# Kernel optimization log

Measured on AMD Instinct MI355X. Metric: run time of the kernel, lower is better.

Reference implementation:

```python
import jax, jax.numpy as jnp
import numpy as np


def setup_inputs() -> dict:
    key = jax.random.key(0)
    k1, k2, k3, k4 = jax.random.split(key, 4)
    b, s, h, z = 4, 4096, 2048, 64
    scale = 1.0 / np.sqrt(h)
    return {
        "hidden_states": jax.random.normal(k1, (b, s, h), dtype=jnp.float32),
        # nn.Linear(h, z, bias=False): store as (h, z) so y = x @ W
        "Wq": jax.random.normal(k2, (h, z), dtype=jnp.float32) * scale,
        "Wk": jax.random.normal(k3, (h, z), dtype=jnp.float32) * scale,
        "Wv": jax.random.normal(k4, (h, z), dtype=jnp.float32) * scale,
    }


def reference(hidden_states, Wq, Wk, Wv):
    b, s, h = hidden_states.shape
    z = Wq.shape[1]
    # Three small projections: (b, s, z), cast to float32 as in original
    q = jnp.einsum("bsh,hz->bsz", hidden_states, Wq).astype(jnp.float32)
    k = jnp.einsum("bsh,hz->bsz", hidden_states, Wk).astype(jnp.float32)
    v = jnp.einsum("bsh,hz->bsz", hidden_states, Wv).astype(jnp.float32)
    # Per-token outer product over the expert dim: (b, s, z, z)
    attn = q[..., :, None] * k[..., None, :]
    attn = jax.nn.softmax(attn, axis=-1)
    # Weighted sum over the key expert axis j: out[..., i] = sum_j attn[..., i, j] * v[..., j]
    out = jnp.einsum("bsij,bsj->bsi", attn, v)
    return out.reshape(b * s, z)
```

## Files before the change

### kernel.cpp

```cpp
#include <hip/hip_runtime.h>


typedef __bf16 bf16x8 __attribute__((ext_vector_type(8)));
typedef float f32x4  __attribute__((ext_vector_type(4)));

#define NTOK   16384
#define HDIM   2048
#define NCHUNK 64
#define KCH    32
#define CH_STRIDE (12 * 2 * 512)

#define SWZ(row, kq) ((kq) ^ ((row) & 7))

#define GLOAD_LDS16(g, l)                                                      \
  __builtin_amdgcn_global_load_lds(                                            \
      (const __attribute__((address_space(1))) void*)(g),                      \
      (__attribute__((address_space(3))) void*)(l), 16, 0, 0)

#define WAITV7 asm volatile("s_waitcnt vmcnt(7)" ::: "memory")
#define WAITV0 asm volatile("s_waitcnt vmcnt(0)" ::: "memory")
#define SBAR   __builtin_amdgcn_s_barrier()
#define SCHEDB __builtin_amdgcn_sched_barrier(0)

__global__ void pack_w_kernel(const float* __restrict__ Wq,
                              const float* __restrict__ Wk,
                              const float* __restrict__ Wv,
                              __bf16* __restrict__ bfrag)
{
  int u = blockIdx.x * blockDim.x + threadIdx.x;
  if (u >= NCHUNK * 12 * 64) return;
  int l  = u & 63;
  int tn = (u >> 6) % 12;
  int c  = u / (12 * 64);
  int n  = tn * 16 + (l & 15);
  int kb = c * 32 + ((l >> 4) << 3);
  const float* W = (n < 64) ? Wq : (n < 128) ? Wk : Wv;
  int nn = n & 63;
  bf16x8 hi, lo;
#pragma unroll
  for (int j = 0; j < 8; ++j) {
    float f = W[(size_t)(kb + j) * 64 + nn];
    __bf16 h = (__bf16)f;
    hi[j] = h;
    lo[j] = (__bf16)(f - (float)h);
  }
  size_t base = (size_t)(c * 12 + tn) * 1024 + (size_t)l * 8;
  *(bf16x8*)(bfrag + base)       = hi;
  *(bf16x8*)(bfrag + base + 512) = lo;
}

#define ASMLOADB(S, cc)                                                        \
  {                                                                            \
    const __bf16* nbp  = bp + (size_t)(cc) * CH_STRIDE;                        \
    const __bf16* nbp4 = nbp + 2048;                                           \
    asm volatile("global_load_dwordx4 %0, %1, off"                             \
                 : "=&v"(S##h[0]) : "v"(nbp)  : "memory");                     \
    asm volatile("global_load_dwordx4 %0, %1, off offset:1024"                 \
                 : "=&v"(S##l[0]) : "v"(nbp)  : "memory");                     \
    asm volatile("global_load_dwordx4 %0, %1, off offset:2048"                 \
                 : "=&v"(S##h[1]) : "v"(nbp)  : "memory");                     \
    asm volatile("global_load_dwordx4 %0, %1, off offset:3072"                 \
                 : "=&v"(S##l[1]) : "v"(nbp)  : "memory");                     \
    asm volatile("global_load_dwordx4 %0, %1, off"                             \
                 : "=&v"(S##h[2]) : "v"(nbp4) : "memory");                     \
    asm volatile("global_load_dwordx4 %0, %1, off offset:1024"                 \
                 : "=&v"(S##l[2]) : "v"(nbp4) : "memory");                     \
  }

#define COMPUTE(ab, S)                                                         \
  {                                                                            \
    const int r0 = mr, r1 = 16 + mr;                                           \
    float4 A[4];                                                               \
    A[0] = *(const float4*)&(ab)[r0 * 32 + SWZ(r0, 2 * quad)     * 4];         \
    A[1] = *(const float4*)&(ab)[r0 * 32 + SWZ(r0, 2 * quad + 1) * 4];         \
    A[2] = *(const float4*)&(ab)[r1 * 32 + SWZ(r1, 2 * quad)     * 4];         \
    A[3] = *(const float4*)&(ab)[r1 * 32 + SWZ(r1, 2 * quad + 1) * 4];         \
    bf16x8 ah[2], al[2];                                                       \
    _Pragma("unroll")                                                          \
    for (int i = 0; i < 2; ++i) {                                              \
      float av[8] = {A[2*i].x, A[2*i].y, A[2*i].z, A[2*i].w,                   \
                     A[2*i+1].x, A[2*i+1].y, A[2*i+1].z, A[2*i+1].w};          \
      _Pragma("unroll")                                                        \
      for (int j = 0; j < 8; ++j) {                                            \
        __bf16 h = (__bf16)av[j];                                              \
        ah[i][j] = h;                                                          \
        al[i][j] = (__bf16)(av[j] - (float)h);                                 \
      }                                                                        \
    }                                                                          \
    _Pragma("unroll")                                                          \
    for (int i = 0; i < 2; ++i)                                                \
      _Pragma("unroll")                                                        \
      for (int t = 0; t < 3; ++t) {                                            \
        acc[i][t] = __builtin_amdgcn_mfma_f32_16x16x32_bf16(ah[i], S##h[t], acc[i][t], 0, 0, 0); \
        acc[i][t] = __builtin_amdgcn_mfma_f32_16x16x32_bf16(al[i], S##h[t], acc[i][t], 0, 0, 0); \
        acc[i][t] = __builtin_amdgcn_mfma_f32_16x16x32_bf16(ah[i], S##l[t], acc[i][t], 0, 0, 0); \
      }                                                                        \
  }

__global__ __launch_bounds__(512, 4) void router_kernel(
    const float* __restrict__ x,
    const __bf16* __restrict__ bfrag,
    float* __restrict__ out)
{
  const int tok0 = blockIdx.x * 32;
  const int w    = threadIdx.x >> 6;
  const int lane = threadIdx.x & 63;
  const int kh   = w >> 2;
  const int wc   = w & 3;
  const int mr   = lane & 15;
  const int quad = lane >> 4;

  __shared__ float qkv[2][32 * 196];
  __shared__ float bufA[2][2][1024];

  const int su   = threadIdx.x & 255;
  const int srow = su >> 3;
  const int skq  = su & 7;
  const float* aSrc = x + (size_t)(tok0 + srow) * HDIM + kh * 1024
                        + SWZ(srow, skq) * 4;
  float* aDst0 = &bufA[kh][0][(w & 3) * 256];
  float* aDst1 = &bufA[kh][1][(w & 3) * 256];

  const __bf16* bp = bfrag + (size_t)(kh * KCH) * CH_STRIDE
                           + (size_t)(3 * wc) * 1024 + (size_t)lane * 8;

  f32x4 acc[2][3];
#pragma unroll
  for (int i = 0; i < 2; ++i)
#pragma unroll
    for (int t = 0; t < 3; ++t)
      acc[i][t] = (f32x4){0.f, 0.f, 0.f, 0.f};

  bf16x8 B0h[3], B0l[3], B1h[3], B1l[3];

  GLOAD_LDS16(aSrc, aDst0);
  ASMLOADB(B0, 0)
  GLOAD_LDS16(aSrc + 32, aDst1);
  ASMLOADB(B1, 1)

  for (int c = 0; c < KCH; c += 2) {
    WAITV7;
    SBAR;
    SCHEDB;
    COMPUTE(bufA[kh][0], B0)
    SBAR;
    if (c + 2 < KCH) {
      GLOAD_LDS16(aSrc + (c + 2) * 32, aDst0);
      ASMLOADB(B0, c + 2)
    }
    if (c + 1 < KCH - 1) { WAITV7; } else { WAITV0; }
    SBAR;
    SCHEDB;
    COMPUTE(bufA[kh][1], B1)
    SBAR;
    if (c + 3 < KCH) {
      GLOAD_LDS16(aSrc + (c + 3) * 32, aDst1);
      ASMLOADB(B1, c + 3)
    }
  }

#pragma unroll
  for (int i = 0; i < 2; ++i)
#pragma unroll
    for (int t = 0; t < 3; ++t) {
      int col = wc * 48 + t * 16 + mr;
      int row = i * 16 + quad * 4;
#pragma unroll
      for (int r = 0; r < 4; ++r)
        qkv[kh][(row + r) * 196 + col] = acc[i][t][r];
    }
  __syncthreads();

  const int tt = threadIdx.x >> 4;
  const int g  = threadIdx.x & 15;
  const float* q0 = qkv[0] + tt * 196;
  const float* q1 = qkv[1] + tt * 196;
  float qs[4], lsum[4], osum[4];
#pragma unroll
  for (int ii = 0; ii < 4; ++ii) {
    qs[ii]   = (q0[g * 4 + ii] + q1[g * 4 + ii]) * 1.44269504f;
    lsum[ii] = 0.f;
    osum[ii] = 0.f;
  }
  for (int j = 0; j < 64; ++j) {
    float kj = q0[64 + j]  + q1[64 + j];
    float vj = q0[128 + j] + q1[128 + j];
#pragma unroll
    for (int ii = 0; ii < 4; ++ii) {
      float e = __builtin_amdgcn_exp2f(qs[ii] * kj);
      lsum[ii] += e;
      osum[ii] = fmaf(e, vj, osum[ii]);
    }
  }
  float4 r0v;
  r0v.x = osum[0] / lsum[0]; r0v.y = osum[1] / lsum[1];
  r0v.z = osum[2] / lsum[2]; r0v.w = osum[3] / lsum[3];
  float* op = out + (size_t)(tok0 + tt) * 64 + g * 4;
  *(float4*)op = r0v;
}

extern "C" void kernel_launch(void* const* d_in, const int* in_sizes, int n_in,
                              void* d_out, int out_size, void* d_ws, size_t ws_size,
                              hipStream_t stream)
{
  const float* x  = (const float*)d_in[0];
  const float* Wq = (const float*)d_in[1];
  const float* Wk = (const float*)d_in[2];
  const float* Wv = (const float*)d_in[3];
  __bf16* bfrag   = (__bf16*)d_ws;
  float*  out     = (float*)d_out;

  pack_w_kernel<<<(NCHUNK * 12 * 64 + 255) / 256, 256, 0, stream>>>(Wq, Wk, Wv, bfrag);
  router_kernel<<<NTOK / 32, 512, 0, stream>>>(x, bfrag, out);
}
```

Baseline: 246.2 us.

## Use a four-slot LDS ring for activation tiles aliased with qkv scratch

The A-tile staging moves from a double buffer to a four-slot ring that reuses the qkv shared array, so A tiles are prefetched two chunk-pairs ahead. The main loop now processes two chunks per barrier pair, halving barriers and using a vmcnt(2) wait instead of vmcnt(7). Aliasing the staging buffers into qkv cuts LDS per block, which could allow more resident blocks per CU. In exchange, the B-fragment register loads are issued after both computes, which shortens their lead time before use.

New measurement: 223.6 us. -9.2%, faster.

```diff
diff --git a/kernel.cpp b/kernel.cpp
--- a/kernel.cpp
+++ b/kernel.cpp
@@ -17,7 +17,7 @@
       (const __attribute__((address_space(1))) void*)(g),                      \
       (__attribute__((address_space(3))) void*)(l), 16, 0, 0)
 
-#define WAITV7 asm volatile("s_waitcnt vmcnt(7)" ::: "memory")
+#define WAITV2 asm volatile("s_waitcnt vmcnt(2)" ::: "memory")
 #define WAITV0 asm volatile("s_waitcnt vmcnt(0)" ::: "memory")
 #define SBAR   __builtin_amdgcn_s_barrier()
 #define SCHEDB __builtin_amdgcn_sched_barrier(0)
@@ -110,16 +110,15 @@
   const int mr   = lane & 15;
   const int quad = lane >> 4;
 
-  __shared__ float qkv[2][32 * 196];
-  __shared__ float bufA[2][2][1024];
+  __shared__ float smem[2][32 * 196];
 
   const int su   = threadIdx.x & 255;
   const int srow = su >> 3;
   const int skq  = su & 7;
   const float* aSrc = x + (size_t)(tok0 + srow) * HDIM + kh * 1024
                         + SWZ(srow, skq) * 4;
-  float* aDst0 = &bufA[kh][0][(w & 3) * 256];
-  float* aDst1 = &bufA[kh][1][(w & 3) * 256];
+#define ABUF(b)  (&smem[kh][(b) * 1024])
+#define ADST(b)  (&smem[kh][(b) * 1024 + (w & 3) * 256])
 
   const __bf16* bp = bfrag + (size_t)(kh * KCH) * CH_STRIDE
                            + (size_t)(3 * wc) * 1024 + (size_t)lane * 8;
@@ -133,30 +132,27 @@
 
   bf16x8 B0h[3], B0l[3], B1h[3], B1l[3];
 
-  GLOAD_LDS16(aSrc, aDst0);
   ASMLOADB(B0, 0)
-  GLOAD_LDS16(aSrc + 32, aDst1);
   ASMLOADB(B1, 1)
+  GLOAD_LDS16(aSrc + 0 * 32, ADST(0));
+  GLOAD_LDS16(aSrc + 1 * 32, ADST(1));
+  GLOAD_LDS16(aSrc + 2 * 32, ADST(2));
+  GLOAD_LDS16(aSrc + 3 * 32, ADST(3));
 
   for (int c = 0; c < KCH; c += 2) {
-    WAITV7;
+    if (c + 2 < KCH) { WAITV2; } else { WAITV0; }
     SBAR;
     SCHEDB;
-    COMPUTE(bufA[kh][0], B0)
+
+    COMPUTE(ABUF(c & 3),       B0)
+    COMPUTE(ABUF((c + 1) & 3), B1)
+
+    if (c + 2 < KCH) ASMLOADB(B0, c + 2)
+    if (c + 3 < KCH) ASMLOADB(B1, c + 3)
+
     SBAR;
-    if (c + 2 < KCH) {
-      GLOAD_LDS16(aSrc + (c + 2) * 32, aDst0);
-      ASMLOADB(B0, c + 2)
-    }
-    if (c + 1 < KCH - 1) { WAITV7; } else { WAITV0; }
-    SBAR;
-    SCHEDB;
-    COMPUTE(bufA[kh][1], B1)
-    SBAR;
-    if (c + 3 < KCH) {
-      GLOAD_LDS16(aSrc + (c + 3) * 32, aDst1);
-      ASMLOADB(B1, c + 3)
-    }
+    if (c + 4 < KCH) GLOAD_LDS16(aSrc + (c + 4) * 32, ADST((c + 4) & 3));
+    if (c + 5 < KCH) GLOAD_LDS16(aSrc + (c + 5) * 32, ADST((c + 5) & 3));
   }
 
 #pragma unroll
@@ -167,14 +163,14 @@
       int row = i * 16 + quad * 4;
 #pragma unroll
       for (int r = 0; r < 4; ++r)
-        qkv[kh][(row + r) * 196 + col] = acc[i][t][r];
+        smem[kh][(row + r) * 196 + col] = acc[i][t][r];
     }
   __syncthreads();
 
   const int tt = threadIdx.x >> 4;
   const int g  = threadIdx.x & 15;
-  const float* q0 = qkv[0] + tt * 196;
-  const float* q1 = qkv[1] + tt * 196;
+  const float* q0 = &smem[0][tt * 196];
+  const float* q1 = &smem[1][tt * 196];
   float qs[4], lsum[4], osum[4];
 #pragma unroll
   for (int ii = 0; ii < 4; ++ii) {
```
